# Optimization experiments

Hardware: AMD Instinct MI355X
Metric: run time of the kernel (lower is better)

Reference implementation:

```python
import jax, jax.numpy as jnp
import numpy as np

# Model hyperparams (must match init_kwargs)
N_CATEGORIES = 1000
EMBED_DIM = 128
N_DEMAND = 8
HIDDEN = 128
B, L, N_ITEMS = 16, 50, 8192


def setup_inputs() -> dict:
    key = jax.random.key(0)
    ks = jax.random.split(key, 12)
    inp = {}
    inp["input"] = jax.random.randint(ks[0], (B, L), 0, N_CATEGORIES)
    inp["candidate_pool_category"] = jax.random.randint(ks[1], (N_ITEMS,), 0, N_CATEGORIES)
    inp["session_last_catgy_index"] = jax.random.randint(ks[2], (B,), 0, L)
    inp["mask_catgy"] = jnp.ones((B, L), dtype=jnp.float32)
    # Learned parameters (torch Linear stored as (in, out) so y = x @ W + b)
    emb = 0.02 * jax.random.normal(ks[3], (N_CATEGORIES, EMBED_DIM), dtype=jnp.float32)
    inp["emb_table"] = emb.at[0].set(0.0)  # padding_idx=0
    sd = 1.0 / np.sqrt(EMBED_DIM)
    sh = 1.0 / np.sqrt(HIDDEN)
    inp["Wd"] = sd * jax.random.normal(ks[4], (EMBED_DIM, N_DEMAND * HIDDEN), dtype=jnp.float32)
    inp["Wk"] = sd * jax.random.normal(ks[5], (EMBED_DIM, HIDDEN), dtype=jnp.float32)
    inp["bk"] = sd * jax.random.normal(ks[6], (HIDDEN,), dtype=jnp.float32)
    inp["W1"] = (1.0 / np.sqrt(2 * HIDDEN)) * jax.random.normal(ks[7], (2 * HIDDEN, HIDDEN), dtype=jnp.float32)
    inp["b1"] = sh * jax.random.normal(ks[8], (HIDDEN,), dtype=jnp.float32)
    inp["w_score"] = sh * jax.random.normal(ks[9], (HIDDEN,), dtype=jnp.float32)
    inp["Wc"] = sh * jax.random.normal(ks[10], (HIDDEN, N_CATEGORIES), dtype=jnp.float32)
    inp["bc"] = sh * jax.random.normal(ks[11], (N_CATEGORIES,), dtype=jnp.float32)
    return inp


def reference(input, candidate_pool_category, session_last_catgy_index, mask_catgy,
              emb_table, Wd, Wk, bk, W1, b1, w_score, Wc, bc):
    B_, L_ = input.shape
    h = Wk.shape[1]
    D = Wd.shape[1] // h

    emb = emb_table[input]                      # (B, L, d)  (dropout = identity at eval)
    emb_cand = emb_table[candidate_pool_category]  # (N, d)

    hidden_key = emb @ Wk + bk                  # (B, L, h)
    hidden_demand = (emb @ Wd).reshape(B_, L_, D, h)
    # demand_agg == 'exp': log(sum(exp(.), axis=seq))
    agg = jax.nn.logsumexp(hidden_demand, axis=1)   # (B, D, h)

    # demand similarity loss: mean off-diagonal cosine similarity between demands
    hn = agg / (jnp.linalg.norm(agg, axis=-1, keepdims=True) + 1e-12)
    sim = jnp.einsum('bdh,beh->bde', hn, hn)
    off = sim * (1.0 - jnp.eye(D, dtype=sim.dtype))
    demand_sim_loss = jnp.sum(off) / (B_ * D * (D - 1))

    hidden_key_cand = emb_cand @ Wk + bk        # (N, h)

    # MLP score: cat([demand, key]) @ W1 == demand @ W1[:h] + key @ W1[h:]
    Wd1, Wk1 = W1[:h], W1[h:]
    pd = agg @ Wd1                              # (B, D, h)
    pk = hidden_key @ Wk1                       # (B, L, h)
    s = jax.nn.relu(pd[:, None, :, :] + pk[:, :, None, :] + b1)  # (B, L, D, h)
    # torch does .view(B, D, L) on a contiguous (B, L, D) tensor -> raw reshape (kept faithful)
    demand_score = (s @ w_score).reshape(B_, D, L_)              # (B, D, L)

    pkc = hidden_key_cand @ Wk1                 # (N, h)
    sc = jax.nn.relu(pd[:, :, None, :] + pkc[None, None, :, :] + b1)  # (B, D, N, h)
    demand_score_candidate = sc @ w_score       # (B, D, N)

    # predict_catgy ('mlp'): linear head over aggregated demand (reconstructed; body truncated in source)
    catgy_score = agg @ Wc + bc                 # (B, D, n_categories)

    return (catgy_score, demand_score, demand_score_candidate, emb, emb_cand, demand_sim_loss)
```

## Files before the change

kernel.cpp:

```cpp
#include <hip/hip_runtime.h>
#include <hip/hip_bf16.h>

#define NB 16
#define NL 50
#define ND 8
#define NH 128
#define NC 1000
#define NI 8192

#define OFF_CAT  0
#define OFF_DS   128000
#define OFF_DSC  134400
#define OFF_EMB  1182976
#define OFF_EMBC 1285376
#define OFF_LOSS 2333952

#define WS_SPART 0
#define WS_PK    81920
#define WS_PKCT  184320
#define WS_WP    1232896
#define WS_BP    1249280
#define WS_AGG   1249408
#define WS_PD2   1265792

__global__ __launch_bounds__(128) void k_prep(
    const float* __restrict__ Wk, const float* __restrict__ bk,
    const float* __restrict__ W1, float* __restrict__ ws_wp,
    float* __restrict__ ws_bp, float* __restrict__ out_loss)
{
    const int t = threadIdx.x;
    const int bxx = blockIdx.x;
    __shared__ float wk_s[256];
    const float* __restrict__ Wk1 = W1 + 128 * 128;
    if (bxx < 64) {
        const int r0 = bxx * 2;
        wk_s[t]       = Wk[r0 * 128 + t];
        wk_s[128 + t] = Wk[(r0 + 1) * 128 + t];
        __syncthreads();
        float a0 = 0.f, a1 = 0.f;
        for (int k = 0; k < 128; k += 4) {
            #pragma unroll
            for (int j = 0; j < 4; ++j) {
                const float w = Wk1[(k + j) * 128 + t];
                a0 = fmaf(wk_s[k + j], w, a0);
                a1 = fmaf(wk_s[128 + k + j], w, a1);
            }
        }
        ws_wp[r0 * 128 + t]       = a0;
        ws_wp[(r0 + 1) * 128 + t] = a1;
    } else {
        wk_s[t] = bk[t];
        __syncthreads();
        float a0 = 0.f;
        for (int k = 0; k < 128; k += 4) {
            #pragma unroll
            for (int j = 0; j < 4; ++j)
                a0 = fmaf(wk_s[k + j], Wk1[(k + j) * 128 + t], a0);
        }
        ws_bp[t] = a0;
        if (t == 0) out_loss[0] = 0.f;
    }
}

__global__ __launch_bounds__(256) void k_main(
    const int* __restrict__ inp, const int* __restrict__ cand,
    const float* __restrict__ emb_table, const float* __restrict__ Wd,
    const float* __restrict__ ws_wp, const float* __restrict__ ws_bp,
    float* __restrict__ out_emb, float* __restrict__ out_embc,
    float* __restrict__ ws_pk, float* __restrict__ ws_pkcT,
    float* __restrict__ ws_spart)
{
    const int bx = blockIdx.x;
    const int t = threadIdx.x;
    const int c = t & 127, g = t >> 7;
    __shared__ __align__(16) float smem[2176];

    if (bx < 100) {
        const int r0 = bx * 8;
        float* e_s = smem;
        #pragma unroll
        for (int r = 0; r < 4; ++r) {
            const int gr = g * 4 + r;
            const int cat = inp[r0 + gr];
            const float v = emb_table[cat * 128 + c];
            e_s[gr * 128 + c] = v;
            out_emb[(r0 + gr) * 128 + c] = v;
        }
        __syncthreads();
        const float bpv = ws_bp[c];
        float acc[4] = {bpv, bpv, bpv, bpv};
        for (int k = 0; k < 128; k += 4) {
            const float w0 = ws_wp[(k + 0) * 128 + c], w1 = ws_wp[(k + 1) * 128 + c];
            const float w2 = ws_wp[(k + 2) * 128 + c], w3 = ws_wp[(k + 3) * 128 + c];
            #pragma unroll
            for (int r = 0; r < 4; ++r) {
                const float4 e4 = *reinterpret_cast<const float4*>(&e_s[(g * 4 + r) * 128 + k]);
                acc[r] = fmaf(e4.w, w3, fmaf(e4.z, w2, fmaf(e4.y, w1, fmaf(e4.x, w0, acc[r]))));
            }
        }
        #pragma unroll
        for (int r = 0; r < 4; ++r) ws_pk[(r0 + g * 4 + r) * 128 + c] = acc[r];
    } else if (bx < 612) {
        const int i0 = (bx - 100) * 16;
        float* e_s = smem;
        #pragma unroll
        for (int r = 0; r < 8; ++r) {
            const int gr = g * 8 + r;
            const int cat = cand[i0 + gr];
            const float v = emb_table[cat * 128 + c];
            e_s[gr * 128 + c] = v;
            out_embc[(i0 + gr) * 128 + c] = v;
        }
        __syncthreads();
        const float bpv = ws_bp[c];
        float acc[8];
        #pragma unroll
        for (int r = 0; r < 8; ++r) acc[r] = bpv;
        for (int k = 0; k < 128; k += 4) {
            const float w0 = ws_wp[(k + 0) * 128 + c], w1 = ws_wp[(k + 1) * 128 + c];
            const float w2 = ws_wp[(k + 2) * 128 + c], w3 = ws_wp[(k + 3) * 128 + c];
            #pragma unroll
            for (int r = 0; r < 8; ++r) {
                const float4 e4 = *reinterpret_cast<const float4*>(&e_s[(g * 8 + r) * 128 + k]);
                acc[r] = fmaf(e4.w, w3, fmaf(e4.z, w2, fmaf(e4.y, w1, fmaf(e4.x, w0, acc[r]))));
            }
        }
        __syncthreads();
        float* tb = smem;
        #pragma unroll
        for (int r = 0; r < 8; ++r) tb[(g * 8 + r) * 132 + c] = acc[r];
        __syncthreads();
        #pragma unroll
        for (int p = 0; p < 2; ++p) {
            const int h = p * 64 + (t >> 2);
            const int ib = (t & 3) * 4;
            const float4 v = make_float4(tb[(ib + 0) * 132 + h], tb[(ib + 1) * 132 + h],
                                         tb[(ib + 2) * 132 + h], tb[(ib + 3) * 132 + h]);
            *reinterpret_cast<float4*>(&ws_pkcT[(size_t)h * NI + i0 + ib]) = v;
        }
    } else {
        const int idx = bx - 612;
        const int bd = idx / 5, chunk = idx % 5;
        const int b = bd >> 3, d = bd & 7;
        const int half = g;
        float* se = smem;
        float* ss = smem + 1280;
        for (int ii = t; ii < 1280; ii += 256) {
            const int row = ii >> 7, col = ii & 127;
            const int cat = inp[b * NL + chunk * 10 + row];
            se[ii] = emb_table[cat * 128 + col];
        }
        __syncthreads();
        const float* __restrict__ wp = Wd + d * 128 + c;
        float acc[5] = {0.f, 0.f, 0.f, 0.f, 0.f};
        const int l0 = half * 5;
        for (int k = 0; k < 128; k += 4) {
            const float w0 = wp[(k + 0) * 1024], w1 = wp[(k + 1) * 1024];
            const float w2 = wp[(k + 2) * 1024], w3 = wp[(k + 3) * 1024];
            #pragma unroll
            for (int li = 0; li < 5; ++li) {
                const float4 e4 = *reinterpret_cast<const float4*>(&se[(l0 + li) * 128 + k]);
                acc[li] = fmaf(e4.w, w3, fmaf(e4.z, w2, fmaf(e4.y, w1, fmaf(e4.x, w0, acc[li]))));
            }
        }
        float s = 0.f;
        #pragma unroll
        for (int li = 0; li < 5; ++li) s += expf(acc[li]);
        ss[half * 128 + c] = s;
        __syncthreads();
        if (half == 0)
            ws_spart[(bd * 5 + chunk) * 128 + c] = ss[c] + ss[128 + c];
    }
}

__global__ __launch_bounds__(256) void k_agg2(
    const float* __restrict__ ws_spart, const float* __restrict__ W1,
    const float* __restrict__ b1, const float* __restrict__ Wc,
    const float* __restrict__ bc, float* __restrict__ ws_agg,
    float* __restrict__ ws_pd2, float* __restrict__ out_cat)
{
    const int bd = blockIdx.x;
    const int t = threadIdx.x;
    const int c = t & 127, half = t >> 7;
    __shared__ __align__(16) float a_s[128];
    if (half == 0) {
        float s = 0.f;
        #pragma unroll
        for (int ch = 0; ch < 5; ++ch) s += ws_spart[(bd * 5 + ch) * 128 + c];
        const float av = logf(s);
        a_s[c] = av;
        ws_agg[bd * 128 + c] = av;
    }
    __syncthreads();
    if (half == 0) {
        float acc = b1[c];
        for (int k = 0; k < 128; k += 4) {
            acc = fmaf(a_s[k + 0], W1[(k + 0) * 128 + c], acc);
            acc = fmaf(a_s[k + 1], W1[(k + 1) * 128 + c], acc);
            acc = fmaf(a_s[k + 2], W1[(k + 2) * 128 + c], acc);
            acc = fmaf(a_s[k + 3], W1[(k + 3) * 128 + c], acc);
        }
        ws_pd2[bd * 128 + c] = acc;
    }
    float acc4[4];
    int   col4[4];
    #pragma unroll
    for (int j = 0; j < 4; ++j) {
        const int col = t + j * 256;
        col4[j] = (col < NC) ? col : (NC - 1);
        acc4[j] = bc[col4[j]];
    }
    for (int k = 0; k < 128; ++k) {
        const float av = a_s[k];
        const float* wr = Wc + (size_t)k * NC;
        #pragma unroll
        for (int j = 0; j < 4; ++j) acc4[j] = fmaf(av, wr[col4[j]], acc4[j]);
    }
    #pragma unroll
    for (int j = 0; j < 4; ++j) {
        const int col = t + j * 256;
        if (col < NC) out_cat[bd * NC + col] = acc4[j];
    }
}

__global__ __launch_bounds__(256) void k_tail3(
    const float* __restrict__ ws_agg, const float* __restrict__ ws_pd2,
    const float* __restrict__ ws_pk, const float* __restrict__ ws_pkcT,
    const float* __restrict__ w_score, float* __restrict__ out_ds,
    float* __restrict__ out_dsc, float* __restrict__ out_loss)
{
    const int bx = blockIdx.x;
    const int t = threadIdx.x;
    __shared__ __align__(16) float smem[928];
    float* pd_s = smem;
    float* ws_s = smem + 512;
    float* sp   = smem + 640;
    float* aux  = smem + 896;

    if (bx < 1024) {
        const int ichunk = bx & 31, rh = (bx >> 5) & 1, b = bx >> 6;
        const int r0 = b * 8 + rh * 4;
        const int i = ichunk * 256 + t;
        for (int j = t; j < 512; j += 256) pd_s[j] = ws_pd2[r0 * 128 + j];
        if (t < 128) ws_s[t] = w_score[t];
        __syncthreads();
        float a0 = 0.f, a1 = 0.f, a2 = 0.f, a3 = 0.f;
        const float* __restrict__ pc0 = ws_pkcT + i;
        float4 pv = make_float4(pc0[0], pc0[NI], pc0[2 * NI], pc0[3 * NI]);
        for (int h = 0; h < 128; h += 4) {
            const float4 cur = pv;
            if (h + 4 < 128) {
                const float* __restrict__ pn = ws_pkcT + (size_t)(h + 4) * NI + i;
                pv = make_float4(pn[0], pn[NI], pn[2 * NI], pn[3 * NI]);
            }
            const float4 w4 = *reinterpret_cast<const float4*>(&ws_s[h]);
            const float4 p0 = *reinterpret_cast<const float4*>(&pd_s[h]);
            const float4 p1 = *reinterpret_cast<const float4*>(&pd_s[128 + h]);
            const float4 p2 = *reinterpret_cast<const float4*>(&pd_s[256 + h]);
            const float4 p3 = *reinterpret_cast<const float4*>(&pd_s[384 + h]);
            a0 = fmaf(fmaxf(p0.x + cur.x, 0.f), w4.x, a0);
            a0 = fmaf(fmaxf(p0.y + cur.y, 0.f), w4.y, a0);
            a0 = fmaf(fmaxf(p0.z + cur.z, 0.f), w4.z, a0);
            a0 = fmaf(fmaxf(p0.w + cur.w, 0.f), w4.w, a0);
            a1 = fmaf(fmaxf(p1.x + cur.x, 0.f), w4.x, a1);
            a1 = fmaf(fmaxf(p1.y + cur.y, 0.f), w4.y, a1);
            a1 = fmaf(fmaxf(p1.z + cur.z, 0.f), w4.z, a1);
            a1 = fmaf(fmaxf(p1.w + cur.w, 0.f), w4.w, a1);
            a2 = fmaf(fmaxf(p2.x + cur.x, 0.f), w4.x, a2);
            a2 = fmaf(fmaxf(p2.y + cur.y, 0.f), w4.y, a2);
            a2 = fmaf(fmaxf(p2.z + cur.z, 0.f), w4.z, a2);
            a2 = fmaf(fmaxf(p2.w + cur.w, 0.f), w4.w, a2);
            a3 = fmaf(fmaxf(p3.x + cur.x, 0.f), w4.x, a3);
            a3 = fmaf(fmaxf(p3.y + cur.y, 0.f), w4.y, a3);
            a3 = fmaf(fmaxf(p3.z + cur.z, 0.f), w4.z, a3);
            a3 = fmaf(fmaxf(p3.w + cur.w, 0.f), w4.w, a3);
        }
        out_dsc[(size_t)(r0 + 0) * NI + i] = a0;
        out_dsc[(size_t)(r0 + 1) * NI + i] = a1;
        out_dsc[(size_t)(r0 + 2) * NI + i] = a2;
        out_dsc[(size_t)(r0 + 3) * NI + i] = a3;
    } else if (bx < 1824) {
        const int bl = bx - 1024;
        const int b = bl / 50, l = bl % 50;
        const int c = t & 127, g = t >> 7;
        const int w = t >> 6, lane = t & 63;
        float* red = aux;
        const float pkv = ws_pk[(size_t)bl * 128 + c];
        const float wv = w_score[c];
        #pragma unroll
        for (int r = 0; r < 4; ++r) {
            const int d = g * 4 + r;
            float v = fmaxf(ws_pd2[(b * 8 + d) * 128 + c] + pkv, 0.f) * wv;
            v += __shfl_down(v, 32); v += __shfl_down(v, 16); v += __shfl_down(v, 8);
            v += __shfl_down(v, 4);  v += __shfl_down(v, 2);  v += __shfl_down(v, 1);
            if (lane == 0) red[w * 4 + r] = v;
        }
        __syncthreads();
        if (t < 8) {
            const int gg = t >> 2, rr = t & 3;
            out_ds[b * 400 + l * 8 + t] = red[(2 * gg) * 4 + rr] + red[(2 * gg + 1) * 4 + rr];
        }
    } else {
        const int b = bx - 1824;
        const int c = t & 127, g = t >> 7;
        const int w = t >> 6, lane = t & 63;
        float* normp = aux;
        float* wred  = aux + 16;
        float a[4];
        #pragma unroll
        for (int r = 0; r < 4; ++r) a[r] = ws_agg[(b * 8 + g * 4 + r) * 128 + c];
        #pragma unroll
        for (int r = 0; r < 4; ++r) {
            float s = a[r] * a[r];
            s += __shfl_down(s, 32); s += __shfl_down(s, 16); s += __shfl_down(s, 8);
            s += __shfl_down(s, 4);  s += __shfl_down(s, 2);  s += __shfl_down(s, 1);
            if (lane == 0) normp[w * 4 + r] = s;
        }
        __syncthreads();
        float Sp = 0.f;
        #pragma unroll
        for (int r = 0; r < 4; ++r) {
            const float nsq = normp[(2 * g) * 4 + r] + normp[(2 * g + 1) * 4 + r];
            const float iv = 1.f / (sqrtf(nsq) + 1e-12f);
            Sp = fmaf(a[r], iv, Sp);
        }
        sp[g * 128 + c] = Sp;
        __syncthreads();
        float p = 0.f;
        if (t < 128) {
            const float S = sp[c] + sp[128 + c];
            p = S * S;
        }
        p += __shfl_down(p, 32); p += __shfl_down(p, 16); p += __shfl_down(p, 8);
        p += __shfl_down(p, 4);  p += __shfl_down(p, 2);  p += __shfl_down(p, 1);
        if (lane == 0) wred[w] = p;
        __syncthreads();
        if (t == 0) {
            float corr = 0.f;
            #pragma unroll
            for (int d = 0; d < 8; ++d) {
                const float nsq = normp[(2 * (d >> 2)) * 4 + (d & 3)] +
                                  normp[(2 * (d >> 2) + 1) * 4 + (d & 3)];
                const float iv = 1.f / (sqrtf(nsq) + 1e-12f);
                corr = fmaf(nsq, iv * iv, corr);
            }
            atomicAdd(out_loss,
                      (wred[0] + wred[1] + wred[2] + wred[3] - corr) * (1.0f / 896.0f));
        }
    }
}

extern "C" void kernel_launch(void* const* d_in, const int* in_sizes, int n_in,
                              void* d_out, int out_size, void* d_ws, size_t ws_size,
                              hipStream_t stream)
{
    const int*   input     = (const int*)d_in[0];
    const int*   cand      = (const int*)d_in[1];
    const float* emb_table = (const float*)d_in[4];
    const float* Wd        = (const float*)d_in[5];
    const float* Wk        = (const float*)d_in[6];
    const float* bk        = (const float*)d_in[7];
    const float* W1        = (const float*)d_in[8];
    const float* b1        = (const float*)d_in[9];
    const float* w_score   = (const float*)d_in[10];
    const float* Wc        = (const float*)d_in[11];
    const float* bc        = (const float*)d_in[12];

    float* out = (float*)d_out;
    float* out_cat  = out + OFF_CAT;
    float* out_ds   = out + OFF_DS;
    float* out_dsc  = out + OFF_DSC;
    float* out_emb  = out + OFF_EMB;
    float* out_embc = out + OFF_EMBC;
    float* out_loss = out + OFF_LOSS;

    float* ws       = (float*)d_ws;
    float* ws_spart = ws + WS_SPART;
    float* ws_pk    = ws + WS_PK;
    float* ws_pkcT  = ws + WS_PKCT;
    float* ws_wp    = ws + WS_WP;
    float* ws_bp    = ws + WS_BP;
    float* ws_agg   = ws + WS_AGG;
    float* ws_pd2   = ws + WS_PD2;

    k_prep<<<65, 128, 0, stream>>>(Wk, bk, W1, ws_wp, ws_bp, out_loss);
    k_main<<<1252, 256, 0, stream>>>(input, cand, emb_table, Wd, ws_wp, ws_bp,
                                     out_emb, out_embc, ws_pk, ws_pkcT, ws_spart);
    k_agg2<<<128, 256, 0, stream>>>(ws_spart, W1, b1, Wc, bc, ws_agg, ws_pd2, out_cat);
    k_tail3<<<1840, 256, 0, stream>>>(ws_agg, ws_pd2, ws_pk, ws_pkcT, w_score,
                                      out_ds, out_dsc, out_loss);
}
```

Before: 128.0 us.

## Regroup kernels into stages to drop one launch and overlap independent work

The demand logsumexp partial-sum blocks move from the main kernel into the prep kernel, and the aggregation/category-head blocks move into the main kernel. This cuts the pipeline from four launches to three and lets independent work run side by side within each stage. The prep work is also remapped to 256-thread blocks, one output row per half-block. In exchange, each fused kernel mixes heterogeneous block types, which can unbalance the block schedule and raise register pressure.

```diff
diff --git a/kernel.cpp b/kernel.cpp
--- a/kernel.cpp
+++ b/kernel.cpp
@@ -23,52 +23,90 @@
 #define WS_AGG   1249408
 #define WS_PD2   1265792
 
-__global__ __launch_bounds__(128) void k_prep(
-    const float* __restrict__ Wk, const float* __restrict__ bk,
-    const float* __restrict__ W1, float* __restrict__ ws_wp,
-    float* __restrict__ ws_bp, float* __restrict__ out_loss)
+__global__ __launch_bounds__(256) void k_stage0(
+    const int* __restrict__ inp, const float* __restrict__ emb_table,
+    const float* __restrict__ Wd, const float* __restrict__ Wk,
+    const float* __restrict__ bk, const float* __restrict__ W1,
+    float* __restrict__ ws_wp, float* __restrict__ ws_bp,
+    float* __restrict__ ws_spart, float* __restrict__ out_loss)
 {
+    const int bx = blockIdx.x;
     const int t = threadIdx.x;
-    const int bxx = blockIdx.x;
-    __shared__ float wk_s[256];
-    const float* __restrict__ Wk1 = W1 + 128 * 128;
-    if (bxx < 64) {
-        const int r0 = bxx * 2;
-        wk_s[t]       = Wk[r0 * 128 + t];
-        wk_s[128 + t] = Wk[(r0 + 1) * 128 + t];
-        __syncthreads();
-        float a0 = 0.f, a1 = 0.f;
+    const int c = t & 127, g = t >> 7;
+    __shared__ __align__(16) float smem[1536];
+
+    if (bx < 64) {
+        float* wk_s = smem;
+        const float* __restrict__ Wk1 = W1 + 128 * 128;
+        const int r0 = bx * 2;
+        wk_s[t] = Wk[(r0 + g) * 128 + c];
+        __syncthreads();
+        float a = 0.f;
         for (int k = 0; k < 128; k += 4) {
             #pragma unroll
-            for (int j = 0; j < 4; ++j) {
-                const float w = Wk1[(k + j) * 128 + t];
-                a0 = fmaf(wk_s[k + j], w, a0);
-                a1 = fmaf(wk_s[128 + k + j], w, a1);
-            }
-        }
-        ws_wp[r0 * 128 + t]       = a0;
-        ws_wp[(r0 + 1) * 128 + t] = a1;
+            for (int j = 0; j < 4; ++j)
+                a = fmaf(wk_s[g * 128 + k + j], Wk1[(k + j) * 128 + c], a);
+        }
+        ws_wp[(r0 + g) * 128 + c] = a;
+    } else if (bx == 64) {
+        float* wk_s = smem;
+        const float* __restrict__ Wk1 = W1 + 128 * 128;
+        if (t < 128) wk_s[t] = bk[t];
+        __syncthreads();
+        if (t < 128) {
+            float a = 0.f;
+            for (int k = 0; k < 128; k += 4) {
+                #pragma unroll
+                for (int j = 0; j < 4; ++j)
+                    a = fmaf(wk_s[k + j], Wk1[(k + j) * 128 + t], a);
+            }
+            ws_bp[t] = a;
+        }
+        if (t == 0) out_loss[0] = 0.f;
     } else {
-        wk_s[t] = bk[t];
-        __syncthreads();
-        float a0 = 0.f;
+        const int idx = bx - 65;
+        const int bd = idx / 5, chunk = idx % 5;
+        const int b = bd >> 3, d = bd & 7;
+        float* se = smem;
+        float* ss = smem + 1280;
+        for (int ii = t; ii < 1280; ii += 256) {
+            const int row = ii >> 7, col = ii & 127;
+            const int cat = inp[b * NL + chunk * 10 + row];
+            se[ii] = emb_table[cat * 128 + col];
+        }
+        __syncthreads();
+        const float* __restrict__ wp = Wd + d * 128 + c;
+        float acc[5] = {0.f, 0.f, 0.f, 0.f, 0.f};
+        const int l0 = g * 5;
         for (int k = 0; k < 128; k += 4) {
-            #pragma unroll
-            for (int j = 0; j < 4; ++j)
-                a0 = fmaf(wk_s[k + j], Wk1[(k + j) * 128 + t], a0);
-        }
-        ws_bp[t] = a0;
-        if (t == 0) out_loss[0] = 0.f;
+            const float w0 = wp[(k + 0) * 1024], w1 = wp[(k + 1) * 1024];
+            const float w2 = wp[(k + 2) * 1024], w3 = wp[(k + 3) * 1024];
+            #pragma unroll
+            for (int li = 0; li < 5; ++li) {
+                const float4 e4 = *reinterpret_cast<const float4*>(&se[(l0 + li) * 128 + k]);
+                acc[li] = fmaf(e4.w, w3, fmaf(e4.z, w2, fmaf(e4.y, w1, fmaf(e4.x, w0, acc[li]))));
+            }
+        }
+        float s = 0.f;
+        #pragma unroll
+        for (int li = 0; li < 5; ++li) s += expf(acc[li]);
+        ss[g * 128 + c] = s;
+        __syncthreads();
+        if (g == 0)
+            ws_spart[(bd * 5 + chunk) * 128 + c] = ss[c] + ss[128 + c];
     }
 }
 
-__global__ __launch_bounds__(256) void k_main(
+__global__ __launch_bounds__(256) void k_stage1(
     const int* __restrict__ inp, const int* __restrict__ cand,
-    const float* __restrict__ emb_table, const float* __restrict__ Wd,
-    const float* __restrict__ ws_wp, const float* __restrict__ ws_bp,
+    const float* __restrict__ emb_table, const float* __restrict__ W1,
+    const float* __restrict__ b1, const float* __restrict__ Wc,
+    const float* __restrict__ bc, const float* __restrict__ ws_wp,
+    const float* __restrict__ ws_bp, const float* __restrict__ ws_spart,
     float* __restrict__ out_emb, float* __restrict__ out_embc,
-    float* __restrict__ ws_pk, float* __restrict__ ws_pkcT,
-    float* __restrict__ ws_spart)
+    float* __restrict__ out_cat, float* __restrict__ ws_pk,
+    float* __restrict__ ws_pkcT, float* __restrict__ ws_agg,
+    float* __restrict__ ws_pd2)
 {
     const int bx = blockIdx.x;
     const int t = threadIdx.x;
@@ -139,87 +177,46 @@
             *reinterpret_cast<float4*>(&ws_pkcT[(size_t)h * NI + i0 + ib]) = v;
         }
     } else {
-        const int idx = bx - 612;
-        const int bd = idx / 5, chunk = idx % 5;
-        const int b = bd >> 3, d = bd & 7;
-        const int half = g;
-        float* se = smem;
-        float* ss = smem + 1280;
-        for (int ii = t; ii < 1280; ii += 256) {
-            const int row = ii >> 7, col = ii & 127;
-            const int cat = inp[b * NL + chunk * 10 + row];
-            se[ii] = emb_table[cat * 128 + col];
-        }
-        __syncthreads();
-        const float* __restrict__ wp = Wd + d * 128 + c;
-        float acc[5] = {0.f, 0.f, 0.f, 0.f, 0.f};
-        const int l0 = half * 5;
-        for (int k = 0; k < 128; k += 4) {
-            const float w0 = wp[(k + 0) * 1024], w1 = wp[(k + 1) * 1024];
-            const float w2 = wp[(k + 2) * 1024], w3 = wp[(k + 3) * 1024];
-            #pragma unroll
-            for (int li = 0; li < 5; ++li) {
-                const float4 e4 = *reinterpret_cast<const float4*>(&se[(l0 + li) * 128 + k]);
-                acc[li] = fmaf(e4.w, w3, fmaf(e4.z, w2, fmaf(e4.y, w1, fmaf(e4.x, w0, acc[li]))));
-            }
-        }
-        float s = 0.f;
-        #pragma unroll
-        for (int li = 0; li < 5; ++li) s += expf(acc[li]);
-        ss[half * 128 + c] = s;
-        __syncthreads();
-        if (half == 0)
-            ws_spart[(bd * 5 + chunk) * 128 + c] = ss[c] + ss[128 + c];
-    }
-}
-
-__global__ __launch_bounds__(256) void k_agg2(
-    const float* __restrict__ ws_spart, const float* __restrict__ W1,
-    const float* __restrict__ b1, const float* __restrict__ Wc,
-    const float* __restrict__ bc, float* __restrict__ ws_agg,
-    float* __restrict__ ws_pd2, float* __restrict__ out_cat)
-{
-    const int bd = blockIdx.x;
-    const int t = threadIdx.x;
-    const int c = t & 127, half = t >> 7;
-    __shared__ __align__(16) float a_s[128];
-    if (half == 0) {
-        float s = 0.f;
-        #pragma unroll
-        for (int ch = 0; ch < 5; ++ch) s += ws_spart[(bd * 5 + ch) * 128 + c];
-        const float av = logf(s);
-        a_s[c] = av;
-        ws_agg[bd * 128 + c] = av;
-    }
-    __syncthreads();
-    if (half == 0) {
-        float acc = b1[c];
-        for (int k = 0; k < 128; k += 4) {
-            acc = fmaf(a_s[k + 0], W1[(k + 0) * 128 + c], acc);
-            acc = fmaf(a_s[k + 1], W1[(k + 1) * 128 + c], acc);
-            acc = fmaf(a_s[k + 2], W1[(k + 2) * 128 + c], acc);
-            acc = fmaf(a_s[k + 3], W1[(k + 3) * 128 + c], acc);
-        }
-        ws_pd2[bd * 128 + c] = acc;
-    }
-    float acc4[4];
-    int   col4[4];
-    #pragma unroll
-    for (int j = 0; j < 4; ++j) {
-        const int col = t + j * 256;
-        col4[j] = (col < NC) ? col : (NC - 1);
-        acc4[j] = bc[col4[j]];
-    }
-    for (int k = 0; k < 128; ++k) {
-        const float av = a_s[k];
-        const float* wr = Wc + (size_t)k * NC;
-        #pragma unroll
-        for (int j = 0; j < 4; ++j) acc4[j] = fmaf(av, wr[col4[j]], acc4[j]);
-    }
-    #pragma unroll
-    for (int j = 0; j < 4; ++j) {
-        const int col = t + j * 256;
-        if (col < NC) out_cat[bd * NC + col] = acc4[j];
+        const int bd = bx - 612;
+        float* a_s = smem;
+        if (g == 0) {
+            float s = 0.f;
+            #pragma unroll
+            for (int ch = 0; ch < 5; ++ch) s += ws_spart[(bd * 5 + ch) * 128 + c];
+            const float av = logf(s);
+            a_s[c] = av;
+            ws_agg[bd * 128 + c] = av;
+        }
+        __syncthreads();
+        if (g == 0) {
+            float acc = b1[c];
+            for (int k = 0; k < 128; k += 4) {
+                acc = fmaf(a_s[k + 0], W1[(k + 0) * 128 + c], acc);
+                acc = fmaf(a_s[k + 1], W1[(k + 1) * 128 + c], acc);
+                acc = fmaf(a_s[k + 2], W1[(k + 2) * 128 + c], acc);
+                acc = fmaf(a_s[k + 3], W1[(k + 3) * 128 + c], acc);
+            }
+            ws_pd2[bd * 128 + c] = acc;
+        }
+        float acc4[4];
+        int   col4[4];
+        #pragma unroll
+        for (int j = 0; j < 4; ++j) {
+            const int col = t + j * 256;
+            col4[j] = (col < NC) ? col : (NC - 1);
+            acc4[j] = bc[col4[j]];
+        }
+        for (int k = 0; k < 128; ++k) {
+            const float av = a_s[k];
+            const float* wr = Wc + (size_t)k * NC;
+            #pragma unroll
+            for (int j = 0; j < 4; ++j) acc4[j] = fmaf(av, wr[col4[j]], acc4[j]);
+        }
+        #pragma unroll
+        for (int j = 0; j < 4; ++j) {
+            const int col = t + j * 256;
+            if (col < NC) out_cat[bd * NC + col] = acc4[j];
+        }
     }
 }
 
@@ -383,10 +380,12 @@
     float* ws_agg   = ws + WS_AGG;
     float* ws_pd2   = ws + WS_PD2;
 
-    k_prep<<<65, 128, 0, stream>>>(Wk, bk, W1, ws_wp, ws_bp, out_loss);
-    k_main<<<1252, 256, 0, stream>>>(input, cand, emb_table, Wd, ws_wp, ws_bp,
-                                     out_emb, out_embc, ws_pk, ws_pkcT, ws_spart);
-    k_agg2<<<128, 256, 0, stream>>>(ws_spart, W1, b1, Wc, bc, ws_agg, ws_pd2, out_cat);
+    k_stage0<<<705, 256, 0, stream>>>(input, emb_table, Wd, Wk, bk, W1,
+                                      ws_wp, ws_bp, ws_spart, out_loss);
+    k_stage1<<<740, 256, 0, stream>>>(input, cand, emb_table, W1, b1, Wc, bc,
+                                      ws_wp, ws_bp, ws_spart,
+                                      out_emb, out_embc, out_cat,
+                                      ws_pk, ws_pkcT, ws_agg, ws_pd2);
     k_tail3<<<1840, 256, 0, stream>>>(ws_agg, ws_pd2, ws_pk, ws_pkcT, w_score,
                                       out_ds, out_dsc, out_loss);
 }
```

New measurement: 119.7 us, median of 2. -6.5%, faster.
